# Kernel optimization log

Hardware: AMD Instinct MI355X
Metric: run time of the kernel (lower is better)

## Reference

```python
import jax, jax.numpy as jnp
import numpy as np
from jax import lax

NH = 8  # heads
BN_EPS = 1e-3


def setup_inputs() -> dict:
    key = jax.random.key(0)
    ks = jax.random.split(key, 8)
    B, C1, H, W = 8, 256, 64, 64
    N, GC, EC = 32, 512, 256
    return {
        "x": jax.random.normal(ks[0], (B, C1, H, W), jnp.float32),
        "guide": jax.random.normal(ks[1], (B, N, GC), jnp.float32),
        "gl_w": jax.random.normal(ks[2], (EC, GC), jnp.float32) * 0.02,
        "gl_b": jax.random.normal(ks[3], (EC,), jnp.float32) * 0.02,
        "attn_bias": jnp.zeros((NH,), jnp.float32),
        "proj_w": jax.random.normal(ks[4], (C1, C1, 3, 3), jnp.float32) * 0.02,
        "bn_gamma": jnp.ones((C1,), jnp.float32),
        "bn_beta": jnp.zeros((C1,), jnp.float32),
        "bn_mean": jax.random.normal(ks[5], (C1,), jnp.float32) * 0.1,
        "bn_var": jax.random.uniform(ks[6], (C1,), jnp.float32, 0.5, 1.5),
    }


def reference(x, guide, gl_w, gl_b, attn_bias, proj_w, bn_gamma, bn_beta, bn_mean, bn_var):
    bs, c1, h, w = x.shape
    hc = c1 // NH
    # guide projection: (B,N,gc) -> (B,N,ec) -> (B,N,nh,hc)
    g = jnp.einsum('bng,eg->bne', guide, gl_w) + gl_b
    g = g.reshape(bs, -1, NH, hc)
    # embed = x (c1 == ec, so no embedding conv)
    emb = x.reshape(bs, NH, hc, h, w)
    # guided scores, max over guides
    aw = jnp.einsum('bmchw,bnmc->bmhwn', emb, g).max(-1)  # (B,nh,H,W)
    aw = jax.nn.sigmoid(aw / jnp.sqrt(jnp.float32(hc)) + attn_bias[None, :, None, None])
    # proj conv: 3x3, stride 1, pad 1, no bias, then BN (eval mode), no act
    p = lax.conv_general_dilated(x, proj_w, (1, 1), ((1, 1), (1, 1)),
                                 dimension_numbers=('NCHW', 'OIHW', 'NCHW'))
    inv = bn_gamma / jnp.sqrt(bn_var + BN_EPS)
    p = p * inv[None, :, None, None] + (bn_beta - bn_mean * inv)[None, :, None, None]
    out = p.reshape(bs, NH, -1, h, w) * aw[:, :, None]
    return out.reshape(bs, -1, h, w)
```

## Files before the change

### kernel.cpp

```cpp
#include <hip/hip_runtime.h>

typedef unsigned short u16;
typedef unsigned int u32;
typedef __bf16 bf16x8 __attribute__((ext_vector_type(8)));
typedef float f32x4 __attribute__((ext_vector_type(4)));

#define OFF_G      0x000000
#define OFF_AW     0x040000
#define OFF_WT     0x140000
#define OFF_SHIFT  0x260000
#define OFF_GLWT   0x261000
#define OFF_XPAD   0x2F0000
#define XPAD_BYTES (8u*66u*66u*256u*2u)
#define WS_NEED    ((size_t)OFF_XPAD + (size_t)XPAD_BYTES)

__device__ __forceinline__ u16 f2bf(float f) {
  union { float f; u32 u; } v; v.f = f;
  return (u16)((v.u + 0x7FFFu + ((v.u >> 16) & 1u)) >> 16);
}

__device__ __forceinline__ void gl2lds16(const u16* g, u16* l) {
  __builtin_amdgcn_global_load_lds(
      (const __attribute__((address_space(1))) void*)g,
      (__attribute__((address_space(3))) void*)l, 16, 0, 0);
}

__global__ __launch_bounds__(256) void prep_k(
    const float* __restrict__ w, const float* __restrict__ gamma,
    const float* __restrict__ beta, const float* __restrict__ mean,
    const float* __restrict__ var, u16* __restrict__ wt, float* __restrict__ shift,
    const float* __restrict__ glw, float* __restrict__ glwT) {
  __shared__ float tile[32][33];
  const int tid = threadIdx.x;
  if (blockIdx.x < 256) {
    const int co = blockIdx.x;
    const float inv = gamma[co] / sqrtf(var[co] + 1e-3f);
    float v[9];
#pragma unroll
    for (int t = 0; t < 9; ++t) v[t] = w[(size_t)co * 2304 + tid * 9 + t];
#pragma unroll
    for (int t = 0; t < 9; ++t) wt[co * 2304 + t * 256 + tid] = f2bf(v[t] * inv);
    if (tid == 0) shift[co] = beta[co] - mean[co] * inv;
  } else {
    const int bid = blockIdx.x - 256;
    const int et = bid >> 4, kt = bid & 15;
    const int row = tid >> 5, col = tid & 31;
#pragma unroll
    for (int r = 0; r < 4; ++r)
      tile[row + r * 8][col] = glw[(size_t)(et * 32 + row + r * 8) * 512 + kt * 32 + col];
    __syncthreads();
#pragma unroll
    for (int r = 0; r < 4; ++r)
      glwT[(size_t)(kt * 32 + row + r * 8) * 256 + et * 32 + col] = tile[col][row + r * 8];
  }
}

__global__ __launch_bounds__(256) void gproj2_k(
    const float* __restrict__ guide, const float* __restrict__ glwT,
    const float* __restrict__ glb, float* __restrict__ g) {
  const int bn = blockIdx.x;
  const int e  = threadIdx.x;
  const float* gd  = guide + (size_t)bn * 512;
  const float* col = glwT + e;
  float acc = glb[e];
#pragma unroll 8
  for (int k = 0; k < 512; ++k)
    acc = fmaf(col[(size_t)k * 256], gd[k], acc);
  g[bn * 256 + e] = acc;
}

__global__ __launch_bounds__(256) void xpaw2_k(const float* __restrict__ x,
                                               const float* __restrict__ g,
                                               const float* __restrict__ bias,
                                               u16* __restrict__ xp,
                                               float* __restrict__ aw) {
  __shared__ u16 tile[256][64];
  __shared__ u16 xT[64][256];
  const int tid = threadIdx.x;
  const int b = blockIdx.x >> 6, y = blockIdx.x & 63;
  const int lane = tid & 63;
  const int wv   = tid >> 6;
  const int l15  = lane & 15;
  const int kq   = lane >> 4;

  bf16x8 af[2][2];
#pragma unroll
  for (int rep = 0; rep < 2; ++rep) {
    const int m = wv + rep * 4;
#pragma unroll
    for (int mi2 = 0; mi2 < 2; ++mi2) {
      const float* ga = g + (size_t)b * 8192 + (mi2 * 16 + l15) * 256 + m * 32 + kq * 8;
      const float4 g0 = *(const float4*)ga;
      const float4 g1 = *(const float4*)(ga + 4);
      u16 tmp[8];
      tmp[0] = f2bf(g0.x); tmp[1] = f2bf(g0.y); tmp[2] = f2bf(g0.z); tmp[3] = f2bf(g0.w);
      tmp[4] = f2bf(g1.x); tmp[5] = f2bf(g1.y); tmp[6] = f2bf(g1.z); tmp[7] = f2bf(g1.w);
      af[rep][mi2] = *(const bf16x8*)tmp;
    }
  }

  {
    const int cb = tid >> 4, xq = tid & 15;
#pragma unroll
    for (int i = 0; i < 16; ++i) {
      const int c = i * 16 + cb;
      const float4 v = *(const float4*)(x + (size_t)(b * 256 + c) * 4096 + y * 64 + xq * 4);
      ushort4 o; o.x = f2bf(v.x); o.y = f2bf(v.y); o.z = f2bf(v.z); o.w = f2bf(v.w);
      *(ushort4*)(&tile[c][xq * 4]) = o;
    }
  }
  __syncthreads();

  const int px = tid & 63, cg = tid >> 6;
  {
    u32 wbuf[32];
#pragma unroll
    for (int j = 0; j < 32; ++j) {
      const u16 lo = tile[cg * 64 + 2 * j][px];
      const u16 hi = tile[cg * 64 + 2 * j + 1][px];
      wbuf[j] = (u32)lo | ((u32)hi << 16);
    }
    u16* dst = xp + ((size_t)(b * 66 + y + 1) * 66 + px + 1) * 256 + cg * 64;
#pragma unroll
    for (int q = 0; q < 8; ++q) {
      uint4 v; v.x = wbuf[q * 4]; v.y = wbuf[q * 4 + 1]; v.z = wbuf[q * 4 + 2]; v.w = wbuf[q * 4 + 3];
      *(uint4*)(dst + q * 8) = v;
      const int slot = (cg * 8 + q) ^ (px & 7);
      *(uint4*)(&xT[px][slot * 8]) = v;
    }
  }
  {
    uint4* rowbase = (uint4*)(xp + (size_t)(b * 66 + y + 1) * 66 * 256);
    if (tid < 32) rowbase[tid] = (uint4){0, 0, 0, 0};
    else if (tid < 64) rowbase[65 * 32 + (tid - 32)] = (uint4){0, 0, 0, 0};
    if (y == 0) {
      uint4* r0 = (uint4*)(xp + (size_t)(b * 66) * 66 * 256);
      for (int i = tid; i < 2112; i += 256) r0[i] = (uint4){0, 0, 0, 0};
    }
    if (y == 63) {
      uint4* r65 = (uint4*)(xp + (size_t)(b * 66 + 65) * 66 * 256);
      for (int i = tid; i < 2112; i += 256) r65[i] = (uint4){0, 0, 0, 0};
    }
  }
  __syncthreads();

#pragma unroll
  for (int rep = 0; rep < 2; ++rep) {
    const int m = wv + rep * 4;
    bf16x8 bfr[4];
#pragma unroll
    for (int ni2 = 0; ni2 < 4; ++ni2) {
      const int row = ni2 * 16 + l15;
      const int slot = (m * 4 + kq) ^ (row & 7);
      bfr[ni2] = *(const bf16x8*)(&xT[row][slot * 8]);
    }
    f32x4 acc[2][4];
#pragma unroll
    for (int i = 0; i < 2; ++i)
#pragma unroll
      for (int j = 0; j < 4; ++j) acc[i][j] = (f32x4){0.f, 0.f, 0.f, 0.f};
#pragma unroll
    for (int mi2 = 0; mi2 < 2; ++mi2)
#pragma unroll
      for (int ni2 = 0; ni2 < 4; ++ni2)
        acc[mi2][ni2] = __builtin_amdgcn_mfma_f32_16x16x32_bf16(af[rep][mi2], bfr[ni2], acc[mi2][ni2], 0, 0, 0);

    const float bm = bias[m];
#pragma unroll
    for (int ni2 = 0; ni2 < 4; ++ni2) {
      float v = acc[0][ni2][0];
#pragma unroll
      for (int j = 1; j < 4; ++j) v = fmaxf(v, acc[0][ni2][j]);
#pragma unroll
      for (int j = 0; j < 4; ++j) v = fmaxf(v, acc[1][ni2][j]);
      v = fmaxf(v, __shfl_xor(v, 16));
      v = fmaxf(v, __shfl_xor(v, 32));
      const float z = v * 0.17677669529663687f + bm;
      const float a = 1.f / (1.f + expf(-z));
      if (kq == 0)
        aw[(size_t)(b * 8 + m) * 4096 + y * 64 + ni2 * 16 + l15] = a;
    }
  }
}

__global__ void attnw_k(const float* __restrict__ x, const float* __restrict__ g,
                        const float* __restrict__ bias, float* __restrict__ aw) {
  const int bm = blockIdx.x;
  const int b = bm >> 3, m = bm & 7;
  const int p = blockIdx.y * 256 + threadIdx.x;
  const float* xp = x + (size_t)(b * 256 + m * 32) * 4096 + p;
  float xv[32];
#pragma unroll
  for (int c = 0; c < 32; ++c) xv[c] = xp[(size_t)c * 4096];
  const float* gv = g + b * 8192 + m * 32;
  float best = -3.4e38f;
#pragma unroll 4
  for (int n = 0; n < 32; ++n) {
    const float* grow = gv + n * 256;
    float s = 0.f;
#pragma unroll
    for (int c = 0; c < 32; ++c) s = fmaf(xv[c], grow[c], s);
    best = fmaxf(best, s);
  }
  const float z = best * 0.17677669529663687f + bias[m];
  aw[(size_t)bm * 4096 + p] = 1.f / (1.f + expf(-z));
}

#define A_U16 8192
#define B_U16 16384
#define BUF_U16 24576

#define STAGE8(koff, bof, ab, bb) do {                                     \
    _Pragma("unroll")                                                      \
    for (int q_ = 0; q_ < 2; ++q_)                                         \
      gl2lds16(awt + (size_t)q_ * 147456 + (koff), (ab) + wv * 512 + q_ * 4096); \
    _Pragma("unroll")                                                      \
    for (int q_ = 0; q_ < 4; ++q_)                                         \
      gl2lds16(bxt + (ptrdiff_t)q_ * 16896 + (bof), (bb) + wv * 512 + q_ * 4096); \
  } while (0)

__global__ __launch_bounds__(512) void conv8c_k(
    const u16* __restrict__ xp, const u16* __restrict__ wt,
    const float* __restrict__ shift, const float* __restrict__ aw,
    float* __restrict__ out) {
  __shared__ u16 lds[3 * BUF_U16];

  const int tid  = threadIdx.x;
  const int lane = tid & 63;
  const int wv   = tid >> 6;
  const int wm   = wv >> 2;
  const int wn   = wv & 3;

  const int pxt = blockIdx.x;
  const int co0 = blockIdx.y * 128;
  const int p0  = pxt * 256;
  const int b   = pxt >> 4;
  const int y0  = (pxt & 15) * 4;

  const int sr    = tid >> 3;
  const int sslot = (tid & 7) ^ (sr & 7);
  const u16* awt = wt + (size_t)(co0 + sr) * 2304 + sslot * 8;
  const u16* bxt = xp + ((size_t)(b * 66 + y0 + 1) * 66 + sr + 1) * 256 + sslot * 8;

  u16* aR  = lds;              u16* bR  = lds + A_U16;
  u16* aN1 = lds + BUF_U16;    u16* bN1 = lds + BUF_U16 + A_U16;
  u16* aN2 = lds + 2*BUF_U16;  u16* bN2 = lds + 2*BUF_U16 + A_U16;

  const int l15 = lane & 15;
  const int sx  = lane & 7;
  const int kq  = lane >> 4;
  const int aRowB = (wm * 64 + l15) * 128;
  const int bRowB = (wn * 64 + l15) * 128;

  f32x4 acc[4][4];
#pragma unroll
  for (int i = 0; i < 4; ++i)
#pragma unroll
    for (int j = 0; j < 4; ++j) acc[i][j] = (f32x4){0.f, 0.f, 0.f, 0.f};

  STAGE8(0,  -17152,      aR,  bR);
  STAGE8(64, -17152 + 64, aN1, bN1);

  int kbase = 0;
  for (int t = 0; t < 9; ++t) {
    const int bof_c = ((t / 3 - 1) * 66 + (t % 3 - 1)) * 256;
    const int t1 = t + 1;
    const int bof_n = (t1 < 9) ? ((t1 / 3 - 1) * 66 + (t1 % 3 - 1)) * 256 : 0;
#pragma unroll
    for (int q = 0; q < 4; ++q) {
      if (t == 8 && q == 3) {
        asm volatile("s_waitcnt vmcnt(0)" ::: "memory");
      } else {
        asm volatile("s_waitcnt vmcnt(6)" ::: "memory");
      }
      __builtin_amdgcn_s_barrier();
      __builtin_amdgcn_sched_barrier(0);

      if ((t < 8) || (q < 2)) {
        const int ksoff = kbase + (q + 2) * 64;
        const int bsoff = (q < 2) ? (bof_c + (q + 2) * 64) : (bof_n + (q - 2) * 64);
        STAGE8(ksoff, bsoff, aN2, bN2);
      }

      const char* Ac = (const char*)aR;
      const char* Bc = (const char*)bR;
#pragma unroll
      for (int ks = 0; ks < 2; ++ks) {
        const int slotb = ((((ks << 2) | kq) ^ sx) << 4);
        bf16x8 af[4], bfr[4];
#pragma unroll
        for (int mi = 0; mi < 4; ++mi)
          af[mi] = *(const bf16x8*)(Ac + aRowB + mi * 2048 + slotb);
#pragma unroll
        for (int ni = 0; ni < 4; ++ni)
          bfr[ni] = *(const bf16x8*)(Bc + bRowB + ni * 2048 + slotb);
        __builtin_amdgcn_s_setprio(1);
#pragma unroll
        for (int mi = 0; mi < 4; ++mi)
#pragma unroll
          for (int ni = 0; ni < 4; ++ni)
            acc[mi][ni] = __builtin_amdgcn_mfma_f32_16x16x32_bf16(af[mi], bfr[ni], acc[mi][ni], 0, 0, 0);
        __builtin_amdgcn_s_setprio(0);
      }

      __builtin_amdgcn_sched_barrier(0);
      __builtin_amdgcn_s_barrier();

      u16* ta = aR; aR = aN1; aN1 = aN2; aN2 = ta;
      u16* tb = bR; bR = bN1; bN1 = bN2; bN2 = tb;
    }
    kbase += 256;
  }

  const int pybase = p0 & 4095;
#pragma unroll
  for (int mi = 0; mi < 4; ++mi) {
#pragma unroll
    for (int j = 0; j < 4; ++j) {
      const int co = co0 + wm * 64 + mi * 16 + ((lane >> 4) << 2) + j;
      const float sh = shift[co];
      const float* awrow = aw + (size_t)(b * 8 + (co >> 5)) * 4096 + pybase;
      float* orow = out + (size_t)(b * 256 + co) * 4096 + pybase;
#pragma unroll
      for (int ni = 0; ni < 4; ++ni) {
        const int pp = wn * 64 + ni * 16 + l15;
        orow[pp] = (acc[mi][ni][j] + sh) * awrow[pp];
      }
    }
  }
}

#define LDK 72
__global__ __launch_bounds__(256) void conv_fb(
    const float* __restrict__ xf, const u16* __restrict__ wt,
    const float* __restrict__ shift, const float* __restrict__ aw,
    float* __restrict__ out) {
  __shared__ u16 As[128 * LDK];
  __shared__ u16 Bs[128 * LDK];
  const int tid  = threadIdx.x;
  const int lane = tid & 63;
  const int wave = tid >> 6;
  const int wm = wave >> 1, wn = wave & 1;
  const int p0  = blockIdx.x * 128;
  const int co0 = blockIdx.y * 128;
  const int b   = p0 >> 12;
  const int y0  = (p0 >> 6) & 63;
  const int bn   = tid & 127;
  const int half = tid >> 7;
  const int py = y0 + (bn >> 6);
  const int px = bn & 63;
  const long xbase = (long)b * (256L * 4096L);
  const int arow0 = tid >> 3;
  const int akc   = tid & 7;

  f32x4 acc[4][4];
#pragma unroll
  for (int i = 0; i < 4; ++i)
#pragma unroll
    for (int j = 0; j < 4; ++j) acc[i][j] = (f32x4){0.f, 0.f, 0.f, 0.f};

  for (int t = 0; t < 9; ++t) {
    const int dy = t / 3 - 1, dxx = t % 3 - 1;
    const int yy = py + dy, xg = px + dxx;
    const bool valid = ((unsigned)yy < 64u) && ((unsigned)xg < 64u);
    const long pixoff = xbase + (long)yy * 64 + xg;
    for (int ci0 = 0; ci0 < 256; ci0 += 64) {
      const int kbase = t * 256 + ci0;
#pragma unroll
      for (int q = 0; q < 4; ++q) {
        const int row = arow0 + q * 32;
        const uint4 v = *(const uint4*)(wt + (size_t)(co0 + row) * 2304 + kbase + akc * 8);
        *(uint4*)(&As[row * LDK + akc * 8]) = v;
      }
      {
        u32 vals[16];
        const int chb = ci0 + half * 32;
#pragma unroll
        for (int jj = 0; jj < 16; ++jj) {
          const float lo = valid ? xf[pixoff + (long)(chb + jj * 2) * 4096] : 0.f;
          const float hi = valid ? xf[pixoff + (long)(chb + jj * 2 + 1) * 4096] : 0.f;
          vals[jj] = (u32)f2bf(lo) | ((u32)f2bf(hi) << 16);
        }
#pragma unroll
        for (int q = 0; q < 4; ++q) {
          uint4 v; v.x = vals[q*4]; v.y = vals[q*4+1]; v.z = vals[q*4+2]; v.w = vals[q*4+3];
          *(uint4*)(&Bs[bn * LDK + half * 32 + q * 8]) = v;
        }
      }
      __syncthreads();
#pragma unroll
      for (int ks = 0; ks < 2; ++ks) {
        const int coloff = ks * 32 + (lane >> 4) * 8;
        bf16x8 af[4], bfr[4];
#pragma unroll
        for (int mi = 0; mi < 4; ++mi)
          af[mi] = *(const bf16x8*)(&As[(wm * 64 + mi * 16 + (lane & 15)) * LDK + coloff]);
#pragma unroll
        for (int ni = 0; ni < 4; ++ni)
          bfr[ni] = *(const bf16x8*)(&Bs[(wn * 64 + ni * 16 + (lane & 15)) * LDK + coloff]);
#pragma unroll
        for (int mi = 0; mi < 4; ++mi)
#pragma unroll
          for (int ni = 0; ni < 4; ++ni)
            acc[mi][ni] = __builtin_amdgcn_mfma_f32_16x16x32_bf16(af[mi], bfr[ni], acc[mi][ni], 0, 0, 0);
      }
      __syncthreads();
    }
  }
  const int pybase = p0 & 4095;
#pragma unroll
  for (int mi = 0; mi < 4; ++mi) {
#pragma unroll
    for (int j = 0; j < 4; ++j) {
      const int co = co0 + wm * 64 + mi * 16 + ((lane >> 4) << 2) + j;
      const float sh = shift[co];
      const float* awrow = aw + (size_t)(b * 8 + (co >> 5)) * 4096 + pybase;
      float* orow = out + (size_t)(b * 256 + co) * 4096 + pybase;
#pragma unroll
      for (int ni = 0; ni < 4; ++ni) {
        const int pp = wn * 64 + ni * 16 + (lane & 15);
        orow[pp] = (acc[mi][ni][j] + sh) * awrow[pp];
      }
    }
  }
}

extern "C" void kernel_launch(void* const* d_in, const int* in_sizes, int n_in,
                              void* d_out, int out_size, void* d_ws, size_t ws_size,
                              hipStream_t stream) {
  (void)in_sizes; (void)n_in; (void)out_size;
  const float* x     = (const float*)d_in[0];
  const float* guide = (const float*)d_in[1];
  const float* glw   = (const float*)d_in[2];
  const float* glb   = (const float*)d_in[3];
  const float* bias  = (const float*)d_in[4];
  const float* pw    = (const float*)d_in[5];
  const float* gamma = (const float*)d_in[6];
  const float* beta  = (const float*)d_in[7];
  const float* mean  = (const float*)d_in[8];
  const float* var   = (const float*)d_in[9];
  float* out = (float*)d_out;

  char* ws = (char*)d_ws;
  float* g     = (float*)(ws + OFF_G);
  float* aw    = (float*)(ws + OFF_AW);
  u16*   wt    = (u16*)(ws + OFF_WT);
  float* shift = (float*)(ws + OFF_SHIFT);
  float* glwT  = (float*)(ws + OFF_GLWT);
  u16*   xpad  = (u16*)(ws + OFF_XPAD);
  const int usexp = (ws_size >= WS_NEED) ? 1 : 0;

  prep_k<<<dim3(384), dim3(256), 0, stream>>>(pw, gamma, beta, mean, var, wt, shift,
                                              glw, glwT);
  gproj2_k<<<dim3(256), dim3(256), 0, stream>>>(guide, glwT, glb, g);
  if (usexp) {
    xpaw2_k<<<dim3(512), dim3(256), 0, stream>>>(x, g, bias, xpad, aw);
    conv8c_k<<<dim3(128, 2), dim3(512), 0, stream>>>(xpad, wt, shift, aw, out);
  } else {
    attnw_k<<<dim3(64, 16), dim3(256), 0, stream>>>(x, g, bias, aw);
    conv_fb<<<dim3(256, 2), dim3(256), 0, stream>>>(x, wt, shift, aw, out);
  }
}
```

Measured before the change: 85.73 us.

## Fuse guide projection into prep kernel using bf16 MFMA, drop transpose

Replaces the separate glw transpose and scalar FMA guide-projection kernels with an MFMA-based bf16 GEMM. It runs inside the same launch as the weight/BN prep blocks, using 32 extra blocks. This removes one kernel launch and the glwT round trip through memory. The guide projection now runs in bf16 instead of fp32, which lowers precision of g (already rounded to bf16 downstream).

```diff
diff --git a/kernel.cpp b/kernel.cpp
--- a/kernel.cpp
+++ b/kernel.cpp
@@ -9,7 +9,6 @@
 #define OFF_AW     0x040000
 #define OFF_WT     0x140000
 #define OFF_SHIFT  0x260000
-#define OFF_GLWT   0x261000
 #define OFF_XPAD   0x2F0000
 #define XPAD_BYTES (8u*66u*66u*256u*2u)
 #define WS_NEED    ((size_t)OFF_XPAD + (size_t)XPAD_BYTES)
@@ -25,12 +24,21 @@
       (__attribute__((address_space(3))) void*)l, 16, 0, 0);
 }
 
-__global__ __launch_bounds__(256) void prep_k(
+__device__ __forceinline__ bf16x8 cvt8(const float* p) {
+  const float4 a = *(const float4*)p;
+  const float4 b = *(const float4*)(p + 4);
+  u16 t[8];
+  t[0] = f2bf(a.x); t[1] = f2bf(a.y); t[2] = f2bf(a.z); t[3] = f2bf(a.w);
+  t[4] = f2bf(b.x); t[5] = f2bf(b.y); t[6] = f2bf(b.z); t[7] = f2bf(b.w);
+  return *(const bf16x8*)t;
+}
+
+__global__ __launch_bounds__(256) void g2_k(
     const float* __restrict__ w, const float* __restrict__ gamma,
     const float* __restrict__ beta, const float* __restrict__ mean,
     const float* __restrict__ var, u16* __restrict__ wt, float* __restrict__ shift,
-    const float* __restrict__ glw, float* __restrict__ glwT) {
-  __shared__ float tile[32][33];
+    const float* __restrict__ guide, const float* __restrict__ glw,
+    const float* __restrict__ glb, float* __restrict__ g) {
   const int tid = threadIdx.x;
   if (blockIdx.x < 256) {
     const int co = blockIdx.x;
@@ -41,32 +49,41 @@
 #pragma unroll
     for (int t = 0; t < 9; ++t) wt[co * 2304 + t * 256 + tid] = f2bf(v[t] * inv);
     if (tid == 0) shift[co] = beta[co] - mean[co] * inv;
-  } else {
-    const int bid = blockIdx.x - 256;
-    const int et = bid >> 4, kt = bid & 15;
-    const int row = tid >> 5, col = tid & 31;
-#pragma unroll
-    for (int r = 0; r < 4; ++r)
-      tile[row + r * 8][col] = glw[(size_t)(et * 32 + row + r * 8) * 512 + kt * 32 + col];
-    __syncthreads();
-#pragma unroll
-    for (int r = 0; r < 4; ++r)
-      glwT[(size_t)(kt * 32 + row + r * 8) * 256 + et * 32 + col] = tile[col][row + r * 8];
-  }
-}
-
-__global__ __launch_bounds__(256) void gproj2_k(
-    const float* __restrict__ guide, const float* __restrict__ glwT,
-    const float* __restrict__ glb, float* __restrict__ g) {
-  const int bn = blockIdx.x;
-  const int e  = threadIdx.x;
-  const float* gd  = guide + (size_t)bn * 512;
-  const float* col = glwT + e;
-  float acc = glb[e];
-#pragma unroll 8
-  for (int k = 0; k < 512; ++k)
-    acc = fmaf(col[(size_t)k * 256], gd[k], acc);
-  g[bn * 256 + e] = acc;
+    return;
+  }
+  const int bid = blockIdx.x - 256;
+  const int b  = bid >> 2;
+  const int e0 = (bid & 3) * 64;
+  const int lane = tid & 63;
+  const int wn   = tid >> 6;
+  const int l15  = lane & 15;
+  const int kq   = lane >> 4;
+
+  const float* ga0 = guide + (size_t)b * 16384 + (size_t)l15 * 512 + kq * 8;
+  const float* gb0 = glw + (size_t)(e0 + wn * 16 + l15) * 512 + kq * 8;
+
+  f32x4 acc[2];
+  acc[0] = (f32x4){0.f, 0.f, 0.f, 0.f};
+  acc[1] = (f32x4){0.f, 0.f, 0.f, 0.f};
+#pragma unroll
+  for (int kc = 0; kc < 16; ++kc) {
+    const int k0 = kc * 32;
+    const bf16x8 bfr = cvt8(gb0 + k0);
+#pragma unroll
+    for (int mi = 0; mi < 2; ++mi) {
+      const bf16x8 af = cvt8(ga0 + (size_t)mi * 16 * 512 + k0);
+      acc[mi] = __builtin_amdgcn_mfma_f32_16x16x32_bf16(af, bfr, acc[mi], 0, 0, 0);
+    }
+  }
+  const int e = e0 + wn * 16 + l15;
+  const float bv = glb[e];
+#pragma unroll
+  for (int mi = 0; mi < 2; ++mi)
+#pragma unroll
+    for (int j = 0; j < 4; ++j) {
+      const int n = mi * 16 + kq * 4 + j;
+      g[(size_t)b * 8192 + n * 256 + e] = acc[mi][j] + bv;
+    }
 }
 
 __global__ __launch_bounds__(256) void xpaw2_k(const float* __restrict__ x,
@@ -88,15 +105,8 @@
   for (int rep = 0; rep < 2; ++rep) {
     const int m = wv + rep * 4;
 #pragma unroll
-    for (int mi2 = 0; mi2 < 2; ++mi2) {
-      const float* ga = g + (size_t)b * 8192 + (mi2 * 16 + l15) * 256 + m * 32 + kq * 8;
-      const float4 g0 = *(const float4*)ga;
-      const float4 g1 = *(const float4*)(ga + 4);
-      u16 tmp[8];
-      tmp[0] = f2bf(g0.x); tmp[1] = f2bf(g0.y); tmp[2] = f2bf(g0.z); tmp[3] = f2bf(g0.w);
-      tmp[4] = f2bf(g1.x); tmp[5] = f2bf(g1.y); tmp[6] = f2bf(g1.z); tmp[7] = f2bf(g1.w);
-      af[rep][mi2] = *(const bf16x8*)tmp;
-    }
+    for (int mi2 = 0; mi2 < 2; ++mi2)
+      af[rep][mi2] = cvt8(g + (size_t)b * 8192 + (mi2 * 16 + l15) * 256 + m * 32 + kq * 8);
   }
 
   {
@@ -446,13 +456,11 @@
   float* aw    = (float*)(ws + OFF_AW);
   u16*   wt    = (u16*)(ws + OFF_WT);
   float* shift = (float*)(ws + OFF_SHIFT);
-  float* glwT  = (float*)(ws + OFF_GLWT);
   u16*   xpad  = (u16*)(ws + OFF_XPAD);
   const int usexp = (ws_size >= WS_NEED) ? 1 : 0;
 
-  prep_k<<<dim3(384), dim3(256), 0, stream>>>(pw, gamma, beta, mean, var, wt, shift,
-                                              glw, glwT);
-  gproj2_k<<<dim3(256), dim3(256), 0, stream>>>(guide, glwT, glb, g);
+  g2_k<<<dim3(288), dim3(256), 0, stream>>>(pw, gamma, beta, mean, var, wt, shift,
+                                            guide, glw, glb, g);
   if (usexp) {
     xpaw2_k<<<dim3(512), dim3(256), 0, stream>>>(x, g, bias, xpad, aw);
     conv8c_k<<<dim3(128, 2), dim3(512), 0, stream>>>(xpad, wt, shift, aw, out);
```

Result: faster. 71.18 us, median of 2 (-17.0%).
